# Performance work log

Hardware: AMD Instinct MI355X
Metric: run time of the kernel (lower is better)

The kernel has to match this reference:

```python
import jax, jax.numpy as jnp
import numpy as np

EPS = 1e-5

def setup_inputs() -> dict:
    key = jax.random.key(0)
    ks = jax.random.split(key, 10)
    B, C, H, W, D = 1, 128, 20, 20, 20
    Cq = C // 8
    s = 0.05
    return {
        "x":   jax.random.normal(ks[0], (B, C, H, W, D), jnp.float32),
        "wq":  jax.random.normal(ks[1], (Cq, C), jnp.float32) * s,
        "bq":  jnp.zeros((Cq,), jnp.float32),
        "wk":  jax.random.normal(ks[2], (Cq, C), jnp.float32) * s,
        "bk":  jnp.zeros((Cq,), jnp.float32),
        "wv":  jax.random.normal(ks[3], (C, C), jnp.float32) * s,
        "bv":  jnp.zeros((C,), jnp.float32),
        "wa":  jax.random.normal(ks[4], (C, C), jnp.float32) * s,
        "ba":  jnp.zeros((C,), jnp.float32),
        "bn_w": jnp.ones((C,), jnp.float32),
        "bn_b": jnp.zeros((C,), jnp.float32),
    }

def reference(x, wq, bq, wk, bk, wv, bv, wa, ba, bn_w, bn_b):
    B, C, H, W, D = x.shape
    N = H * W * D
    xf = x.reshape(B, C, N)                                   # (B,C,N)
    # 1x1 conv projections = per-position channel matmuls
    q = jnp.einsum('oc,bcn->bno', wq, xf) + bq                # (B,N,Cq)
    k = jnp.einsum('oc,bcn->bon', wk, xf) + bk[:, None]       # (B,Cq,N)
    v = jnp.einsum('oc,bcn->bon', wv, xf) + bv[:, None]       # (B,C,N)
    # raw (unscaled) attention, softmax over key positions
    att = jax.nn.softmax(jnp.einsum('bnc,bcm->bnm', q, k), axis=-1)  # (B,N,N)
    # att_value[b,c,i] = sum_j value[b,c,j] * att[b,i,j]
    av = jnp.einsum('bcj,bij->bci', v, att)                   # (B,C,N)
    y = jnp.einsum('oc,bcn->bon', wa, av) + ba[:, None]       # (B,C,N)
    # BatchNorm (training mode): per-channel stats over batch + spatial
    mean = jnp.mean(y, axis=(0, 2), keepdims=True)
    var = jnp.var(y, axis=(0, 2), keepdims=True)
    y = (y - mean) * jax.lax.rsqrt(var + EPS) * bn_w[:, None] + bn_b[:, None]
    out = jax.nn.relu(y) + xf
    return out.reshape(B, C, H, W, D)
```

## Files before the change

kernel.cpp:

```cpp
#include <hip/hip_runtime.h>
#include <math.h>

#define N_POS 8000
#define C_CH  128
#define KSPLIT 5
#define KT_PER 25
#define QTILES 125

typedef __bf16 bf16x8 __attribute__((ext_vector_type(8)));
typedef float  f32x4  __attribute__((ext_vector_type(4)));

#define MFMA(a,b,c) __builtin_amdgcn_mfma_f32_16x16x32_bf16((a),(b),(c),0,0,0)


#define GLOAD_LDS(gp, lp) \
    __builtin_amdgcn_global_load_lds( \
        (const __attribute__((address_space(1))) void*)(gp), \
        (__attribute__((address_space(3))) void*)(lp), 16, 0, 0)

__global__ __launch_bounds__(256) void qkv_kernel(
    const float* __restrict__ x,
    const float* __restrict__ wq, const float* __restrict__ bq,
    const float* __restrict__ wk, const float* __restrict__ bk,
    const float* __restrict__ wv, const float* __restrict__ bv,
    __bf16* __restrict__ q_bf, __bf16* __restrict__ k_bf, __bf16* __restrict__ v_bf)
{
    __shared__ __bf16 x_lds[32 * 136];
    __shared__ __bf16 v_out[128 * 36];

    const int t    = threadIdx.x;
    const int n0   = blockIdx.x * 32;
    const int lane = t & 63;
    const int w    = t >> 6;
    const int l15  = lane & 15;
    const int quad = lane >> 4;

    for (int r = 0; r < 4; ++r) {
        int f = r * 256 + t;
        int ch = f >> 3, n4 = f & 7;
        float4 xv = *reinterpret_cast<const float4*>(&x[ch * N_POS + n0 + n4 * 4]);
        x_lds[(n4 * 4 + 0) * 136 + ch] = (__bf16)xv.x;
        x_lds[(n4 * 4 + 1) * 136 + ch] = (__bf16)xv.y;
        x_lds[(n4 * 4 + 2) * 136 + ch] = (__bf16)xv.z;
        x_lds[(n4 * 4 + 3) * 136 + ch] = (__bf16)xv.w;
    }

    bf16x8 aw[3][4];
    f32x4  acc[3][2];
    const int nmt = (w < 2) ? 3 : 2;
    for (int mi = 0; mi < nmt; ++mi) {
        int mt = w + 4 * mi;
        const float *wrow, *brow;
        if (mt == 0)      { wrow = wq + l15 * 128;               brow = bq; }
        else if (mt == 1) { wrow = wk + l15 * 128;               brow = bk; }
        else              { wrow = wv + ((mt - 2) * 16 + l15) * 128;
                            brow = bv + (mt - 2) * 16; }
        for (int ks = 0; ks < 4; ++ks) {
            float4 f0 = *reinterpret_cast<const float4*>(wrow + ks * 32 + quad * 8);
            float4 f1 = *reinterpret_cast<const float4*>(wrow + ks * 32 + quad * 8 + 4);
            bf16x8 a;
            a[0]=(__bf16)f0.x; a[1]=(__bf16)f0.y; a[2]=(__bf16)f0.z; a[3]=(__bf16)f0.w;
            a[4]=(__bf16)f1.x; a[5]=(__bf16)f1.y; a[6]=(__bf16)f1.z; a[7]=(__bf16)f1.w;
            aw[mi][ks] = a;
        }
        for (int ni = 0; ni < 2; ++ni) {
            acc[mi][ni][0] = brow[quad * 4 + 0]; acc[mi][ni][1] = brow[quad * 4 + 1];
            acc[mi][ni][2] = brow[quad * 4 + 2]; acc[mi][ni][3] = brow[quad * 4 + 3];
        }
    }
    __syncthreads();

    for (int ks = 0; ks < 4; ++ks) {
        bf16x8 b0 = *reinterpret_cast<const bf16x8*>(&x_lds[(0  + l15) * 136 + ks * 32 + quad * 8]);
        bf16x8 b1 = *reinterpret_cast<const bf16x8*>(&x_lds[(16 + l15) * 136 + ks * 32 + quad * 8]);
        for (int mi = 0; mi < nmt; ++mi) {
            acc[mi][0] = MFMA(aw[mi][ks], b0, acc[mi][0]);
            acc[mi][1] = MFMA(aw[mi][ks], b1, acc[mi][1]);
        }
    }

    union S4 { short4 s; __bf16 b[4]; };
    for (int mi = 0; mi < nmt; ++mi) {
        int mt = w + 4 * mi;
        for (int ni = 0; ni < 2; ++ni) {
            S4 u;
            u.b[0]=(__bf16)acc[mi][ni][0]; u.b[1]=(__bf16)acc[mi][ni][1];
            u.b[2]=(__bf16)acc[mi][ni][2]; u.b[3]=(__bf16)acc[mi][ni][3];
            int n = n0 + ni * 16 + l15;
            if (mt == 0) {
                *reinterpret_cast<short4*>(&q_bf[n * 16 + quad * 4]) = u.s;
            } else if (mt == 1) {
                *reinterpret_cast<short4*>(&k_bf[n * 16 + quad * 4]) = u.s;
            } else {
                int ch0 = (mt - 2) * 16 + quad * 4;
                int nl  = ni * 16 + l15;
                v_out[(ch0 + 0) * 36 + nl] = u.b[0];
                v_out[(ch0 + 1) * 36 + nl] = u.b[1];
                v_out[(ch0 + 2) * 36 + nl] = u.b[2];
                v_out[(ch0 + 3) * 36 + nl] = u.b[3];
            }
        }
    }
    __syncthreads();
    for (int r = 0; r < 4; ++r) {
        int f = r * 256 + t;
        int ch = f >> 3, n4 = f & 7;
        int2 d = *reinterpret_cast<const int2*>(&v_out[ch * 36 + n4 * 4]);
        *reinterpret_cast<int2*>(&v_bf[ch * N_POS + n0 + n4 * 4]) = d;
    }
}

__global__ __launch_bounds__(256, 3) void attn_kernel(
    const __bf16* __restrict__ q_bf, const __bf16* __restrict__ k_bf,
    const __bf16* __restrict__ v_bf, float* __restrict__ av_part,
    float* __restrict__ l_part)
{
    __shared__ __bf16 v_buf[2][8192];
    __shared__ __bf16 k_buf[2][1024];
    __shared__ __bf16 p_lds[4096];

    const int t    = threadIdx.x;
    const int qt   = blockIdx.x % QTILES;
    const int sp   = blockIdx.x / QTILES;
    const int n0q  = qt * 64;
    const int lane = t & 63;
    const int w    = t >> 6;
    const int l15  = lane & 15;
    const int quad = lane >> 4;

    const int chL   = lane >> 3;
    const int vpart = (lane & 7) ^ chL;
    const int kkey  = lane >> 1;
    const int khalf = lane & 1;

    bf16x8 aq[4];
    for (int ni = 0; ni < 4; ++ni) {
        for (int j = 0; j < 8; ++j) aq[ni][j] = (__bf16)0.0f;
        if (quad < 2)
            aq[ni] = *reinterpret_cast<const bf16x8*>(
                &q_bf[(n0q + ni * 16 + l15) * 16 + quad * 8]);
    }
    bf16x8 ones;
    for (int j = 0; j < 8; ++j) ones[j] = (__bf16)1.0f;

    f32x4 acc[2][4];
    for (int mi = 0; mi < 2; ++mi)
        for (int ni = 0; ni < 4; ++ni)
            for (int r = 0; r < 4; ++r) acc[mi][ni][r] = 0.f;
    f32x4 lacc;
    for (int r = 0; r < 4; ++r) lacc[r] = 0.f;

    const int kt0 = sp * KT_PER;

    auto stage = [&](int kt, int buf) {
        const int n0k = kt * 64;
        for (int r = 0; r < 4; ++r) {
            int R = w * 4 + r;
            GLOAD_LDS(v_bf + (8 * R + chL) * N_POS + n0k + vpart * 8,
                      &v_buf[buf][R * 512]);
        }
        if (w < 2)
            GLOAD_LDS(k_bf + (size_t)(n0k + w * 32 + kkey) * 16 + khalf * 8,
                      &k_buf[buf][w * 512]);
    };

    stage(kt0, 0);

    const int oS  = w * 2 + (quad >> 1);
    const int sub = (quad & 1) * 4;

    union S4 { short4 sh; __bf16 b[4]; };

    for (int kt = kt0; kt < kt0 + KT_PER; ++kt) {
        const int cur = (kt - kt0) & 1;
        __syncthreads();

        if (kt + 1 < kt0 + KT_PER) stage(kt + 1, cur ^ 1);

        bf16x8 ak;
        for (int j = 0; j < 8; ++j) ak[j] = (__bf16)0.0f;
        if (quad < 2)
            ak = *reinterpret_cast<const bf16x8*>(
                &k_buf[cur][(w * 16 + l15) * 16 + quad * 8]);
#pragma unroll
        for (int ni = 0; ni < 4; ++ni) {
            f32x4 s;
            for (int r = 0; r < 4; ++r) s[r] = 0.f;
            s = MFMA(ak, aq[ni], s);
            S4 u;
            u.b[0] = (__bf16)__expf(s[0]); u.b[1] = (__bf16)__expf(s[1]);
            u.b[2] = (__bf16)__expf(s[2]); u.b[3] = (__bf16)__expf(s[3]);
            *reinterpret_cast<short4*>(
                &p_lds[(oS * 64 + ni * 16 + l15) * 8 + sub]) = u.sh;
        }

        asm volatile("s_waitcnt lgkmcnt(0)" ::: "memory");
        __builtin_amdgcn_s_barrier();
        asm volatile("" ::: "memory");
        __builtin_amdgcn_sched_barrier(0);

        const int chl = l15 & 7;
#pragma unroll
        for (int ks = 0; ks < 2; ++ks) {
            int pz = ((ks * 4 + quad) ^ chl);
            bf16x8 a0 = *reinterpret_cast<const bf16x8*>(
                &v_buf[cur][(((2 * w)     * 2 + (l15 >> 3)) * 64 + chl * 8 + pz) * 8]);
            bf16x8 a1 = *reinterpret_cast<const bf16x8*>(
                &v_buf[cur][(((2 * w + 1) * 2 + (l15 >> 3)) * 64 + chl * 8 + pz) * 8]);
            const int ob = (ks * 4 + quad) * 64;
            bf16x8 p0 = *reinterpret_cast<const bf16x8*>(&p_lds[(ob +  0 + l15) * 8]);
            bf16x8 p1 = *reinterpret_cast<const bf16x8*>(&p_lds[(ob + 16 + l15) * 8]);
            bf16x8 p2 = *reinterpret_cast<const bf16x8*>(&p_lds[(ob + 32 + l15) * 8]);
            bf16x8 p3 = *reinterpret_cast<const bf16x8*>(&p_lds[(ob + 48 + l15) * 8]);
            acc[0][0] = MFMA(a0, p0, acc[0][0]);
            acc[0][1] = MFMA(a0, p1, acc[0][1]);
            acc[0][2] = MFMA(a0, p2, acc[0][2]);
            acc[0][3] = MFMA(a0, p3, acc[0][3]);
            acc[1][0] = MFMA(a1, p0, acc[1][0]);
            acc[1][1] = MFMA(a1, p1, acc[1][1]);
            acc[1][2] = MFMA(a1, p2, acc[1][2]);
            acc[1][3] = MFMA(a1, p3, acc[1][3]);
            bf16x8 pw = *reinterpret_cast<const bf16x8*>(&p_lds[(ob + w * 16 + l15) * 8]);
            lacc = MFMA(ones, pw, lacc);
        }
    }

    float* dst = av_part + (size_t)sp * 1024000;
    for (int mi = 0; mi < 2; ++mi)
        for (int ni = 0; ni < 4; ++ni) {
            int n  = n0q + ni * 16 + l15;
            int ch = (2 * w + mi) * 16 + quad * 4;
            *reinterpret_cast<f32x4*>(&dst[n * 128 + ch]) = acc[mi][ni];
        }
    if (quad == 0)
        l_part[sp * N_POS + n0q + w * 16 + l15] = lacc[0];
}

__global__ __launch_bounds__(256) void proj_out_kernel(
    const float* __restrict__ av_part, const float* __restrict__ l_part,
    const float* __restrict__ wa, const float* __restrict__ ba,
    float* __restrict__ y_ws, float* __restrict__ bn_sum, float* __restrict__ bn_sumsq)
{
    __shared__ __bf16 b_lds[4096];

    const int t    = threadIdx.x;
    const int n0   = blockIdx.x * 32;
    const int lane = t & 63;
    const int w    = t >> 6;
    const int l15  = lane & 15;
    const int quad = lane >> 4;

    for (int r = 0; r < 2; ++r) {
        int g = r * 256 + t;
        int n = g >> 4, oc = g & 15;
        float l = 0.f;
#pragma unroll
        for (int s = 0; s < KSPLIT; ++s) l += l_part[s * N_POS + n0 + n];
        float4 a0 = make_float4(0.f, 0.f, 0.f, 0.f);
        float4 a1 = make_float4(0.f, 0.f, 0.f, 0.f);
#pragma unroll
        for (int s = 0; s < KSPLIT; ++s) {
            const float* p = av_part + (size_t)s * 1024000 + (n0 + n) * 128 + oc * 8;
            float4 u = *reinterpret_cast<const float4*>(p);
            float4 v = *reinterpret_cast<const float4*>(p + 4);
            a0.x += u.x; a0.y += u.y; a0.z += u.z; a0.w += u.w;
            a1.x += v.x; a1.y += v.y; a1.z += v.z; a1.w += v.w;
        }
        float inv = 1.f / l;
        union { int4 iv; __bf16 b[8]; } u;
        u.b[0]=(__bf16)(a0.x*inv); u.b[1]=(__bf16)(a0.y*inv);
        u.b[2]=(__bf16)(a0.z*inv); u.b[3]=(__bf16)(a0.w*inv);
        u.b[4]=(__bf16)(a1.x*inv); u.b[5]=(__bf16)(a1.y*inv);
        u.b[6]=(__bf16)(a1.z*inv); u.b[7]=(__bf16)(a1.w*inv);
        int A = (n >> 4) * 16 + oc;
        int slot = (n & 15) ^ (oc & 7);
        *reinterpret_cast<int4*>(&b_lds[(A * 16 + slot) * 8]) = u.iv;
    }

    bf16x8 aw[2][4];
    f32x4  acc[2][2];
    for (int mi = 0; mi < 2; ++mi) {
        int mt = 2 * w + mi;
        const float* wrow = wa + (mt * 16 + l15) * 128;
        for (int ks = 0; ks < 4; ++ks) {
            float4 f0 = *reinterpret_cast<const float4*>(wrow + ks * 32 + quad * 8);
            float4 f1 = *reinterpret_cast<const float4*>(wrow + ks * 32 + quad * 8 + 4);
            bf16x8 a;
            a[0]=(__bf16)f0.x; a[1]=(__bf16)f0.y; a[2]=(__bf16)f0.z; a[3]=(__bf16)f0.w;
            a[4]=(__bf16)f1.x; a[5]=(__bf16)f1.y; a[6]=(__bf16)f1.z; a[7]=(__bf16)f1.w;
            aw[mi][ks] = a;
        }
        for (int ni = 0; ni < 2; ++ni) {
            acc[mi][ni][0] = ba[mt * 16 + quad * 4 + 0];
            acc[mi][ni][1] = ba[mt * 16 + quad * 4 + 1];
            acc[mi][ni][2] = ba[mt * 16 + quad * 4 + 2];
            acc[mi][ni][3] = ba[mt * 16 + quad * 4 + 3];
        }
    }
    __syncthreads();

    for (int ks = 0; ks < 4; ++ks) {
        int oc = ks * 4 + quad;
        int slot = l15 ^ (oc & 7);
        bf16x8 b0 = *reinterpret_cast<const bf16x8*>(&b_lds[((0  + oc) * 16 + slot) * 8]);
        bf16x8 b1 = *reinterpret_cast<const bf16x8*>(&b_lds[((16 + oc) * 16 + slot) * 8]);
        for (int mi = 0; mi < 2; ++mi) {
            acc[mi][0] = MFMA(aw[mi][ks], b0, acc[mi][0]);
            acc[mi][1] = MFMA(aw[mi][ks], b1, acc[mi][1]);
        }
    }

    for (int mi = 0; mi < 2; ++mi) {
        for (int r = 0; r < 4; ++r) {
            int ch = (2 * w + mi) * 16 + quad * 4 + r;
            float v0 = acc[mi][0][r];
            float v1 = acc[mi][1][r];
            y_ws[ch * N_POS + n0 + 0  + l15] = v0;
            y_ws[ch * N_POS + n0 + 16 + l15] = v1;
            float s1 = v0 + v1;
            float s2 = v0 * v0 + v1 * v1;
#pragma unroll
            for (int off = 8; off >= 1; off >>= 1) {
                s1 += __shfl_xor(s1, off, 64);
                s2 += __shfl_xor(s2, off, 64);
            }
            if (l15 == 0) {
                atomicAdd(&bn_sum[ch],   s1);
                atomicAdd(&bn_sumsq[ch], s2);
            }
        }
    }
}

__global__ __launch_bounds__(256) void bn_relu_kernel(
    const float* __restrict__ y_ws, const float* __restrict__ x,
    const float* __restrict__ bn_sum, const float* __restrict__ bn_sumsq,
    const float* __restrict__ bn_w, const float* __restrict__ bn_b,
    float* __restrict__ out)
{
    const int i4 = blockIdx.x * 256 + threadIdx.x;
    const int c  = i4 / 2000;
    const float mean  = bn_sum[c]   * (1.f / 8000.f);
    const float var   = bn_sumsq[c] * (1.f / 8000.f) - mean * mean;
    const float rstd  = rsqrtf(var + 1e-5f);
    const float scale = bn_w[c] * rstd;
    const float shift = bn_b[c] - mean * scale;

    float4 y4 = reinterpret_cast<const float4*>(y_ws)[i4];
    float4 x4 = reinterpret_cast<const float4*>(x)[i4];
    float4 o4;
    o4.x = fmaxf(y4.x * scale + shift, 0.f) + x4.x;
    o4.y = fmaxf(y4.y * scale + shift, 0.f) + x4.y;
    o4.z = fmaxf(y4.z * scale + shift, 0.f) + x4.z;
    o4.w = fmaxf(y4.w * scale + shift, 0.f) + x4.w;
    reinterpret_cast<float4*>(out)[i4] = o4;
}

extern "C" void kernel_launch(void* const* d_in, const int* in_sizes, int n_in,
                              void* d_out, int out_size, void* d_ws, size_t ws_size,
                              hipStream_t stream)
{
    const float* x    = (const float*)d_in[0];
    const float* wq   = (const float*)d_in[1];
    const float* bq   = (const float*)d_in[2];
    const float* wk   = (const float*)d_in[3];
    const float* bk   = (const float*)d_in[4];
    const float* wv   = (const float*)d_in[5];
    const float* bv   = (const float*)d_in[6];
    const float* wa   = (const float*)d_in[7];
    const float* ba   = (const float*)d_in[8];
    const float* bn_w = (const float*)d_in[9];
    const float* bn_b = (const float*)d_in[10];
    float* out = (float*)d_out;

    char* base = (char*)d_ws;
    float*  av_part = (float*)base;
    __bf16* q_bf    = (__bf16*)(base + 20480000);
    __bf16* k_bf    = (__bf16*)(base + 20736000);
    __bf16* v_bf    = (__bf16*)(base + 20992000);
    float*  l_part  = (float*)(base + 23040000);
    float*  bn_sum   = (float*)(base + 23200000);
    float*  bn_sumsq = bn_sum + 128;
    float*  y_ws    = (float*)(base + 23201024);

    hipMemsetAsync(bn_sum, 0, 1024, stream);
    qkv_kernel<<<250, 256, 0, stream>>>(x, wq, bq, wk, bk, wv, bv, q_bf, k_bf, v_bf);
    attn_kernel<<<QTILES * KSPLIT, 256, 0, stream>>>(q_bf, k_bf, v_bf, av_part, l_part);
    proj_out_kernel<<<250, 256, 0, stream>>>(av_part, l_part, wa, ba, y_ws, bn_sum, bn_sumsq);
    bn_relu_kernel<<<1000, 256, 0, stream>>>(y_ws, x, bn_sum, bn_sumsq, bn_w, bn_b, out);
}
```

Baseline: 161.2 us.

## Load V directly into registers, double-buffer P tile, compute row sums via shuffles

The attention kernel stops staging V and K tiles through LDS with global_load_lds. Each wave now loads its V fragments straight from global memory into registers, and K for the next tile is prefetched into a register. The P tile becomes double-buffered in LDS with an XOR swizzle, so only one barrier is needed per key tile. The softmax denominator is now built from wave shuffles plus a final cross-wave LDS reduction instead of an extra MFMA against ones. The warp tiling also changes to 2 channel-groups × 2 query halves. This reduces LDS traffic and barriers, but global loads become less coalesced and use more registers, and latency hiding now depends on register prefetch within each iteration.

```diff
diff --git a/kernel.cpp b/kernel.cpp
--- a/kernel.cpp
+++ b/kernel.cpp
@@ -12,11 +12,6 @@
 
 #define MFMA(a,b,c) __builtin_amdgcn_mfma_f32_16x16x32_bf16((a),(b),(c),0,0,0)
 
-
-#define GLOAD_LDS(gp, lp) \
-    __builtin_amdgcn_global_load_lds( \
-        (const __attribute__((address_space(1))) void*)(gp), \
-        (__attribute__((address_space(3))) void*)(lp), 16, 0, 0)
 
 __global__ __launch_bounds__(256) void qkv_kernel(
     const float* __restrict__ x,
@@ -115,9 +110,7 @@
     const __bf16* __restrict__ v_bf, float* __restrict__ av_part,
     float* __restrict__ l_part)
 {
-    __shared__ __bf16 v_buf[2][8192];
-    __shared__ __bf16 k_buf[2][1024];
-    __shared__ __bf16 p_lds[4096];
+    __shared__ __bf16 p_lds[2][4096];
 
     const int t    = threadIdx.x;
     const int qt   = blockIdx.x % QTILES;
@@ -127,11 +120,8 @@
     const int w    = t >> 6;
     const int l15  = lane & 15;
     const int quad = lane >> 4;
-
-    const int chL   = lane >> 3;
-    const int vpart = (lane & 7) ^ chL;
-    const int kkey  = lane >> 1;
-    const int khalf = lane & 1;
+    const int wc   = w >> 1;
+    const int wq   = w & 1;
 
     bf16x8 aq[4];
     for (int ni = 0; ni < 4; ++ni) {
@@ -140,100 +130,107 @@
             aq[ni] = *reinterpret_cast<const bf16x8*>(
                 &q_bf[(n0q + ni * 16 + l15) * 16 + quad * 8]);
     }
-    bf16x8 ones;
-    for (int j = 0; j < 8; ++j) ones[j] = (__bf16)1.0f;
-
-    f32x4 acc[2][4];
-    for (int mi = 0; mi < 2; ++mi)
-        for (int ni = 0; ni < 4; ++ni)
-            for (int r = 0; r < 4; ++r) acc[mi][ni][r] = 0.f;
-    f32x4 lacc;
-    for (int r = 0; r < 4; ++r) lacc[r] = 0.f;
-
-    const int kt0 = sp * KT_PER;
-
-    auto stage = [&](int kt, int buf) {
+
+    f32x4 acc[4][2];
+    for (int ct = 0; ct < 4; ++ct)
+        for (int qi = 0; qi < 2; ++qi)
+            for (int r = 0; r < 4; ++r) acc[ct][qi][r] = 0.f;
+    float lp[4] = {0.f, 0.f, 0.f, 0.f};
+
+    const int kt0  = sp * KT_PER;
+    const int ktEnd = kt0 + KT_PER;
+
+    const __bf16* vbase = v_bf + (wc * 64 + l15) * N_POS + quad * 8;
+
+    const int pw_off = l15 * 128 + (((w * 2 + (quad >> 1)) ^ (l15 & 7)) * 16)
+                     + (quad & 1) * 8;
+    int pr_off[2][2];
+    for (int qi = 0; qi < 2; ++qi)
+        for (int ks = 0; ks < 2; ++ks)
+            pr_off[qi][ks] = (wq * 32 + qi * 16 + l15) * 128
+                           + (((ks * 4 + quad) ^ (l15 & 7)) * 16);
+
+    union S4 { short4 sh; __bf16 b[4]; };
+
+    bf16x8 kA, kB;
+    for (int j = 0; j < 8; ++j) { kA[j] = (__bf16)0.0f; kB[j] = (__bf16)0.0f; }
+    if (quad < 2)
+        kA = *reinterpret_cast<const bf16x8*>(
+            &k_bf[(kt0 * 64 + w * 16 + l15) * 16 + quad * 8]);
+
+    auto iter = [&](int kt, bf16x8& kc, bf16x8& kn, int pbuf) {
         const int n0k = kt * 64;
-        for (int r = 0; r < 4; ++r) {
-            int R = w * 4 + r;
-            GLOAD_LDS(v_bf + (8 * R + chL) * N_POS + n0k + vpart * 8,
-                      &v_buf[buf][R * 512]);
-        }
-        if (w < 2)
-            GLOAD_LDS(k_bf + (size_t)(n0k + w * 32 + kkey) * 16 + khalf * 8,
-                      &k_buf[buf][w * 512]);
-    };
-
-    stage(kt0, 0);
-
-    const int oS  = w * 2 + (quad >> 1);
-    const int sub = (quad & 1) * 4;
-
-    union S4 { short4 sh; __bf16 b[4]; };
-
-    for (int kt = kt0; kt < kt0 + KT_PER; ++kt) {
-        const int cur = (kt - kt0) & 1;
-        __syncthreads();
-
-        if (kt + 1 < kt0 + KT_PER) stage(kt + 1, cur ^ 1);
-
-        bf16x8 ak;
-        for (int j = 0; j < 8; ++j) ak[j] = (__bf16)0.0f;
-        if (quad < 2)
-            ak = *reinterpret_cast<const bf16x8*>(
-                &k_buf[cur][(w * 16 + l15) * 16 + quad * 8]);
+        bf16x8 vf[4][2];
+#pragma unroll
+        for (int ct = 0; ct < 4; ++ct)
+#pragma unroll
+            for (int ks = 0; ks < 2; ++ks)
+                vf[ct][ks] = *reinterpret_cast<const bf16x8*>(
+                    vbase + ct * (16 * N_POS) + n0k + ks * 32);
+        if (kt + 1 < ktEnd) {
+            if (quad < 2)
+                kn = *reinterpret_cast<const bf16x8*>(
+                    &k_bf[((n0k + 64) + w * 16 + l15) * 16 + quad * 8]);
+        }
+
+        char* pb = reinterpret_cast<char*>(&p_lds[pbuf][0]);
 #pragma unroll
         for (int ni = 0; ni < 4; ++ni) {
             f32x4 s;
             for (int r = 0; r < 4; ++r) s[r] = 0.f;
-            s = MFMA(ak, aq[ni], s);
+            s = MFMA(kc, aq[ni], s);
             S4 u;
             u.b[0] = (__bf16)__expf(s[0]); u.b[1] = (__bf16)__expf(s[1]);
             u.b[2] = (__bf16)__expf(s[2]); u.b[3] = (__bf16)__expf(s[3]);
-            *reinterpret_cast<short4*>(
-                &p_lds[(oS * 64 + ni * 16 + l15) * 8 + sub]) = u.sh;
-        }
-
-        asm volatile("s_waitcnt lgkmcnt(0)" ::: "memory");
-        __builtin_amdgcn_s_barrier();
-        asm volatile("" ::: "memory");
-        __builtin_amdgcn_sched_barrier(0);
-
-        const int chl = l15 & 7;
+            *reinterpret_cast<short4*>(pb + pw_off + ni * 2048) = u.sh;
+            float ps = (float)u.b[0] + (float)u.b[1]
+                     + (float)u.b[2] + (float)u.b[3];
+            ps += __shfl_xor(ps, 16, 64);
+            ps += __shfl_xor(ps, 32, 64);
+            lp[ni] += ps;
+        }
+
+        __syncthreads();
+
+        const char* pr = reinterpret_cast<const char*>(&p_lds[pbuf][0]);
 #pragma unroll
         for (int ks = 0; ks < 2; ++ks) {
-            int pz = ((ks * 4 + quad) ^ chl);
-            bf16x8 a0 = *reinterpret_cast<const bf16x8*>(
-                &v_buf[cur][(((2 * w)     * 2 + (l15 >> 3)) * 64 + chl * 8 + pz) * 8]);
-            bf16x8 a1 = *reinterpret_cast<const bf16x8*>(
-                &v_buf[cur][(((2 * w + 1) * 2 + (l15 >> 3)) * 64 + chl * 8 + pz) * 8]);
-            const int ob = (ks * 4 + quad) * 64;
-            bf16x8 p0 = *reinterpret_cast<const bf16x8*>(&p_lds[(ob +  0 + l15) * 8]);
-            bf16x8 p1 = *reinterpret_cast<const bf16x8*>(&p_lds[(ob + 16 + l15) * 8]);
-            bf16x8 p2 = *reinterpret_cast<const bf16x8*>(&p_lds[(ob + 32 + l15) * 8]);
-            bf16x8 p3 = *reinterpret_cast<const bf16x8*>(&p_lds[(ob + 48 + l15) * 8]);
-            acc[0][0] = MFMA(a0, p0, acc[0][0]);
-            acc[0][1] = MFMA(a0, p1, acc[0][1]);
-            acc[0][2] = MFMA(a0, p2, acc[0][2]);
-            acc[0][3] = MFMA(a0, p3, acc[0][3]);
-            acc[1][0] = MFMA(a1, p0, acc[1][0]);
-            acc[1][1] = MFMA(a1, p1, acc[1][1]);
-            acc[1][2] = MFMA(a1, p2, acc[1][2]);
-            acc[1][3] = MFMA(a1, p3, acc[1][3]);
-            bf16x8 pw = *reinterpret_cast<const bf16x8*>(&p_lds[(ob + w * 16 + l15) * 8]);
-            lacc = MFMA(ones, pw, lacc);
-        }
-    }
+            bf16x8 p0 = *reinterpret_cast<const bf16x8*>(pr + pr_off[0][ks]);
+            bf16x8 p1 = *reinterpret_cast<const bf16x8*>(pr + pr_off[1][ks]);
+#pragma unroll
+            for (int ct = 0; ct < 4; ++ct) {
+                acc[ct][0] = MFMA(vf[ct][ks], p0, acc[ct][0]);
+                acc[ct][1] = MFMA(vf[ct][ks], p1, acc[ct][1]);
+            }
+        }
+    };
+
+    for (int i = 0; i < KT_PER; i += 2) {
+        iter(kt0 + i, kA, kB, 0);
+        if (i + 1 < KT_PER) iter(kt0 + i + 1, kB, kA, 1);
+    }
+
+    __syncthreads();
+    float* lsh = reinterpret_cast<float*>(&p_lds[0][0]);
+    if (quad == 0) {
+#pragma unroll
+        for (int ni = 0; ni < 4; ++ni)
+            lsh[w * 64 + ni * 16 + l15] = lp[ni];
+    }
+    __syncthreads();
 
     float* dst = av_part + (size_t)sp * 1024000;
-    for (int mi = 0; mi < 2; ++mi)
-        for (int ni = 0; ni < 4; ++ni) {
-            int n  = n0q + ni * 16 + l15;
-            int ch = (2 * w + mi) * 16 + quad * 4;
-            *reinterpret_cast<f32x4*>(&dst[n * 128 + ch]) = acc[mi][ni];
-        }
-    if (quad == 0)
-        l_part[sp * N_POS + n0q + w * 16 + l15] = lacc[0];
+#pragma unroll
+    for (int ct = 0; ct < 4; ++ct)
+#pragma unroll
+        for (int qi = 0; qi < 2; ++qi) {
+            int n  = n0q + wq * 32 + qi * 16 + l15;
+            int ch = wc * 64 + ct * 16 + quad * 4;
+            *reinterpret_cast<f32x4*>(&dst[n * 128 + ch]) = acc[ct][qi];
+        }
+    if (t < 64)
+        l_part[sp * N_POS + n0q + t] =
+            lsh[t] + lsh[64 + t] + lsh[128 + t] + lsh[192 + t];
 }
 
 __global__ __launch_bounds__(256) void proj_out_kernel(
```

Result: slower. 204.2 us (+26.7%).

## Double-buffer P tile, load K via registers, compute row sums in registers

Applied to the files above, without the earlier changes.

The attention loop now double-buffers the probability tile in LDS so one of the two barriers per key tile can be dropped. K is read straight from global memory into registers one tile ahead, and only the V loads still go through LDS, waited on with an explicit vmcnt count. The softmax denominator, previously an extra MFMA against a ones vector, is now accumulated in registers and reduced across lanes and waves at the end. This cuts per-iteration synchronisation and MFMA work, but the hand-tuned vmcnt count and the single barrier make correctness depend on the exact number of in-flight loads, and LDS use rises slightly.

```diff
diff --git a/kernel.cpp b/kernel.cpp
--- a/kernel.cpp
+++ b/kernel.cpp
@@ -116,8 +116,7 @@
     float* __restrict__ l_part)
 {
     __shared__ __bf16 v_buf[2][8192];
-    __shared__ __bf16 k_buf[2][1024];
-    __shared__ __bf16 p_lds[4096];
+    __shared__ __bf16 p_lds[2][4096];
 
     const int t    = threadIdx.x;
     const int qt   = blockIdx.x % QTILES;
@@ -130,8 +129,6 @@
 
     const int chL   = lane >> 3;
     const int vpart = (lane & 7) ^ chL;
-    const int kkey  = lane >> 1;
-    const int khalf = lane & 1;
 
     bf16x8 aq[4];
     for (int ni = 0; ni < 4; ++ni) {
@@ -140,78 +137,86 @@
             aq[ni] = *reinterpret_cast<const bf16x8*>(
                 &q_bf[(n0q + ni * 16 + l15) * 16 + quad * 8]);
     }
-    bf16x8 ones;
-    for (int j = 0; j < 8; ++j) ones[j] = (__bf16)1.0f;
 
     f32x4 acc[2][4];
     for (int mi = 0; mi < 2; ++mi)
         for (int ni = 0; ni < 4; ++ni)
             for (int r = 0; r < 4; ++r) acc[mi][ni][r] = 0.f;
-    f32x4 lacc;
-    for (int r = 0; r < 4; ++r) lacc[r] = 0.f;
-
-    const int kt0 = sp * KT_PER;
-
-    auto stage = [&](int kt, int buf) {
+    float lp[4] = {0.f, 0.f, 0.f, 0.f};
+
+    const int kt0   = sp * KT_PER;
+    const int ktEnd = kt0 + KT_PER;
+
+    auto stageV = [&](int kt) {
         const int n0k = kt * 64;
+        __bf16* vb = &v_buf[kt & 1][0];
         for (int r = 0; r < 4; ++r) {
             int R = w * 4 + r;
             GLOAD_LDS(v_bf + (8 * R + chL) * N_POS + n0k + vpart * 8,
-                      &v_buf[buf][R * 512]);
-        }
-        if (w < 2)
-            GLOAD_LDS(k_bf + (size_t)(n0k + w * 32 + kkey) * 16 + khalf * 8,
-                      &k_buf[buf][w * 512]);
+                      &vb[R * 512]);
+        }
     };
 
-    stage(kt0, 0);
+    bf16x8 kA, kB;
+    for (int j = 0; j < 8; ++j) { kA[j] = (__bf16)0.0f; kB[j] = (__bf16)0.0f; }
+
+    stageV(kt0);
+    if (quad < 2)
+        kA = *reinterpret_cast<const bf16x8*>(
+            &k_bf[(size_t)(kt0 * 64 + w * 16 + l15) * 16 + quad * 8]);
 
     const int oS  = w * 2 + (quad >> 1);
     const int sub = (quad & 1) * 4;
 
     union S4 { short4 sh; __bf16 b[4]; };
 
-    for (int kt = kt0; kt < kt0 + KT_PER; ++kt) {
-        const int cur = (kt - kt0) & 1;
-        __syncthreads();
-
-        if (kt + 1 < kt0 + KT_PER) stage(kt + 1, cur ^ 1);
-
-        bf16x8 ak;
-        for (int j = 0; j < 8; ++j) ak[j] = (__bf16)0.0f;
-        if (quad < 2)
-            ak = *reinterpret_cast<const bf16x8*>(
-                &k_buf[cur][(w * 16 + l15) * 16 + quad * 8]);
+    auto iter = [&](int kt, bf16x8& kc, bf16x8& kn, int pbuf) {
+        const bool last = (kt + 1 >= ktEnd);
+        if (!last) {
+            stageV(kt + 1);
+            if (quad < 2)
+                kn = *reinterpret_cast<const bf16x8*>(
+                    &k_bf[(size_t)((kt + 1) * 64 + w * 16 + l15) * 16 + quad * 8]);
+            asm volatile("s_waitcnt vmcnt(5)" ::: "memory");
+        } else {
+            asm volatile("s_waitcnt vmcnt(0)" ::: "memory");
+        }
+        __builtin_amdgcn_sched_barrier(0);
+
+        __bf16* pb = &p_lds[pbuf][0];
 #pragma unroll
         for (int ni = 0; ni < 4; ++ni) {
             f32x4 s;
             for (int r = 0; r < 4; ++r) s[r] = 0.f;
-            s = MFMA(ak, aq[ni], s);
+            s = MFMA(kc, aq[ni], s);
             S4 u;
             u.b[0] = (__bf16)__expf(s[0]); u.b[1] = (__bf16)__expf(s[1]);
             u.b[2] = (__bf16)__expf(s[2]); u.b[3] = (__bf16)__expf(s[3]);
             *reinterpret_cast<short4*>(
-                &p_lds[(oS * 64 + ni * 16 + l15) * 8 + sub]) = u.sh;
+                &pb[(oS * 64 + ni * 16 + l15) * 8 + sub]) = u.sh;
+            lp[ni] += (float)u.b[0] + (float)u.b[1]
+                    + (float)u.b[2] + (float)u.b[3];
         }
 
         asm volatile("s_waitcnt lgkmcnt(0)" ::: "memory");
         __builtin_amdgcn_s_barrier();
-        asm volatile("" ::: "memory");
         __builtin_amdgcn_sched_barrier(0);
 
+        const __bf16* vb = &v_buf[kt & 1][0];
+        const __bf16* pr = &p_lds[pbuf][0];
         const int chl = l15 & 7;
 #pragma unroll
         for (int ks = 0; ks < 2; ++ks) {
             int pz = ((ks * 4 + quad) ^ chl);
             bf16x8 a0 = *reinterpret_cast<const bf16x8*>(
-                &v_buf[cur][(((2 * w)     * 2 + (l15 >> 3)) * 64 + chl * 8 + pz) * 8]);
+                &vb[(((2 * w)     * 2 + (l15 >> 3)) * 64 + chl * 8 + pz) * 8]);
             bf16x8 a1 = *reinterpret_cast<const bf16x8*>(
-                &v_buf[cur][(((2 * w + 1) * 2 + (l15 >> 3)) * 64 + chl * 8 + pz) * 8]);
+                &vb[(((2 * w + 1) * 2 + (l15 >> 3)) * 64 + chl * 8 + pz) * 8]);
             const int ob = (ks * 4 + quad) * 64;
-            bf16x8 p0 = *reinterpret_cast<const bf16x8*>(&p_lds[(ob +  0 + l15) * 8]);
-            bf16x8 p1 = *reinterpret_cast<const bf16x8*>(&p_lds[(ob + 16 + l15) * 8]);
-            bf16x8 p2 = *reinterpret_cast<const bf16x8*>(&p_lds[(ob + 32 + l15) * 8]);
-            bf16x8 p3 = *reinterpret_cast<const bf16x8*>(&p_lds[(ob + 48 + l15) * 8]);
+            bf16x8 p0 = *reinterpret_cast<const bf16x8*>(&pr[(ob +  0 + l15) * 8]);
+            bf16x8 p1 = *reinterpret_cast<const bf16x8*>(&pr[(ob + 16 + l15) * 8]);
+            bf16x8 p2 = *reinterpret_cast<const bf16x8*>(&pr[(ob + 32 + l15) * 8]);
+            bf16x8 p3 = *reinterpret_cast<const bf16x8*>(&pr[(ob + 48 + l15) * 8]);
             acc[0][0] = MFMA(a0, p0, acc[0][0]);
             acc[0][1] = MFMA(a0, p1, acc[0][1]);
             acc[0][2] = MFMA(a0, p2, acc[0][2]);
@@ -220,10 +225,30 @@
             acc[1][1] = MFMA(a1, p1, acc[1][1]);
             acc[1][2] = MFMA(a1, p2, acc[1][2]);
             acc[1][3] = MFMA(a1, p3, acc[1][3]);
-            bf16x8 pw = *reinterpret_cast<const bf16x8*>(&p_lds[(ob + w * 16 + l15) * 8]);
-            lacc = MFMA(ones, pw, lacc);
-        }
-    }
+        }
+    };
+
+    for (int i = 0; i < KT_PER; i += 2) {
+        iter(kt0 + i, kA, kB, 0);
+        if (i + 1 < KT_PER) iter(kt0 + i + 1, kB, kA, 1);
+    }
+
+    __syncthreads();
+    float* lsh = reinterpret_cast<float*>(&p_lds[0][0]);
+    float lt[4];
+#pragma unroll
+    for (int ni = 0; ni < 4; ++ni) {
+        float ps = lp[ni];
+        ps += __shfl_xor(ps, 16, 64);
+        ps += __shfl_xor(ps, 32, 64);
+        lt[ni] = ps;
+    }
+    if (quad == 0) {
+#pragma unroll
+        for (int ni = 0; ni < 4; ++ni)
+            lsh[w * 64 + ni * 16 + l15] = lt[ni];
+    }
+    __syncthreads();
 
     float* dst = av_part + (size_t)sp * 1024000;
     for (int mi = 0; mi < 2; ++mi)
@@ -232,8 +257,9 @@
             int ch = (2 * w + mi) * 16 + quad * 4;
             *reinterpret_cast<f32x4*>(&dst[n * 128 + ch]) = acc[mi][ni];
         }
-    if (quad == 0)
-        l_part[sp * N_POS + n0q + w * 16 + l15] = lacc[0];
+    if (t < 64)
+        l_part[sp * N_POS + n0q + t] =
+            lsh[t] + lsh[64 + t] + lsh[128 + t] + lsh[192 + t];
 }
 
 __global__ __launch_bounds__(256) void proj_out_kernel(
```

Result: no change. 163.3 us (+1.3%).
